# Optimization experiments

Hardware: AMD Instinct MI355X
Metric: run time of the kernel (lower is better)

The kernel has to match this reference:

```python
import jax, jax.numpy as jnp
import numpy as np

EPS = 1e-8
N_NODES, N_EDGES = 10000, 160000
SI, VI = 128, 16          # node scalar / vector channels
ES, EV = 32, 4            # edge scalar / vector channels
SO, VO = 128, 16          # output scalar / vector channels
MSI, MVI = 2 * SI + ES, 2 * VI + EV   # message input dims: 288, 36
H1 = max(MVI, VO)         # layer-1 hidden = 36 (bottleneck=1)
H2 = max(VO, VO)          # layer-2 hidden = 16
SVO = 3                   # scalarization_vectorization_output_dim


def _safe_norm(x, axis):
    return jnp.sqrt(jnp.sum(x * x, axis=axis) + EPS)


def _gcp(s, v, frames, Wdown, Wdf, Wso, bso, Wup, Wg, bg):
    """GCP block on edge-level inputs (node_inputs=False, vector_gate=True).
    s: [E, si], v: [E, vi, 3], frames: [E, 3, 3]."""
    v_pre = jnp.swapaxes(v, -1, -2)                 # [E, 3, vi]
    v_hid = v_pre @ Wdown                           # [E, 3, h]
    v_norm = _safe_norm(v_hid, axis=-2)             # [E, h]
    v_frames = v_pre @ Wdf                          # [E, 3, svo]
    # scalarize: frames @ v_frames -> [E,3,svo], transpose -> [E,svo,3], flatten to 9
    local = jnp.swapaxes(frames @ v_frames, -1, -2).reshape(v.shape[0], 3 * SVO)
    merged = jnp.concatenate([s, v_norm, local], axis=-1)
    s_out = merged @ Wso + bso                      # [E, so]
    v_out = jnp.swapaxes(v_hid @ Wup, -1, -2)       # [E, vo, 3]
    gate = jax.nn.sigmoid(jax.nn.silu(s_out) @ Wg + bg)  # vector gate
    v_out = v_out * gate[..., None]
    return jax.nn.silu(s_out), v_out


def _lin(key, fan_in, fan_out):
    return jax.random.normal(key, (fan_in, fan_out), dtype=jnp.float32) / np.sqrt(fan_in)


def setup_inputs() -> dict:
    key = jax.random.key(0)
    ks = jax.random.split(key, 24)
    M1 = H1 + MSI + 3 * SVO   # 333
    M2 = H2 + SO + 3 * SVO    # 153
    return {
        "node_s": jax.random.normal(ks[0], (N_NODES, SI), dtype=jnp.float32),
        "node_v": jax.random.normal(ks[1], (N_NODES, VI, 3), dtype=jnp.float32),
        "edge_s": jax.random.normal(ks[2], (N_EDGES, ES), dtype=jnp.float32),
        "edge_v": jax.random.normal(ks[3], (N_EDGES, EV, 3), dtype=jnp.float32),
        "frames": jax.random.normal(ks[4], (N_EDGES, 3, 3), dtype=jnp.float32),
        "g1_Wdown": _lin(ks[5], MVI, H1),
        "g1_Wdf": _lin(ks[6], MVI, SVO),
        "g1_Wso": _lin(ks[7], M1, SO),
        "g1_bso": jnp.zeros((SO,), dtype=jnp.float32),
        "g1_Wup": _lin(ks[8], H1, VO),
        "g1_Wg": _lin(ks[9], SO, VO),
        "g1_bg": jnp.zeros((VO,), dtype=jnp.float32),
        "g2_Wdown": _lin(ks[10], VO, H2),
        "g2_Wdf": _lin(ks[11], VO, SVO),
        "g2_Wso": _lin(ks[12], M2, SO),
        "g2_bso": jnp.zeros((SO,), dtype=jnp.float32),
        "g2_Wup": _lin(ks[13], H2, VO),
        "g2_Wg": _lin(ks[14], SO, VO),
        "g2_bg": jnp.zeros((VO,), dtype=jnp.float32),
        "att_W": _lin(ks[15], SO, 1),
        "att_b": jnp.zeros((1,), dtype=jnp.float32),
        "edge_index": jax.random.randint(ks[16], (2, N_EDGES), 0, N_NODES, dtype=jnp.int64),
    }


def reference(node_s, node_v, edge_s, edge_v, frames,
              g1_Wdown, g1_Wdf, g1_Wso, g1_bso, g1_Wup, g1_Wg, g1_bg,
              g2_Wdown, g2_Wdf, g2_Wso, g2_bso, g2_Wup, g2_Wg, g2_bg,
              att_W, att_b, edge_index):
    row, col = edge_index[0], edge_index[1]
    # edge gather: concat source node, edge, dest node features
    ms = jnp.concatenate([node_s[row], edge_s, node_s[col]], axis=-1)   # [E, 288]
    mv = jnp.concatenate([node_v[row], edge_v, node_v[col]], axis=1)    # [E, 36, 3]
    # message_fusion[0]
    s, v = _gcp(ms, mv, frames, g1_Wdown, g1_Wdf, g1_Wso, g1_bso, g1_Wup, g1_Wg, g1_bg)
    # message_fusion[1] with residual
    s2, v2 = _gcp(s, v, frames, g2_Wdown, g2_Wdf, g2_Wso, g2_bso, g2_Wup, g2_Wg, g2_bg)
    s, v = s + s2, v + v2
    # scalar message attention
    attn = jax.nn.sigmoid(s @ att_W + att_b)
    s = s * attn
    # flatten ScalarVector and scatter-sum aggregate to destination nodes
    flat = jnp.concatenate([s, v.reshape(v.shape[0], VO * 3)], axis=-1)  # [E, 176]
    agg = jax.ops.segment_sum(flat, row, num_segments=N_NODES)           # [N, 176]
    return agg
```

## Files before the change

### kernel.cpp

```cpp
#include <hip/hip_runtime.h>
#include <hip/hip_bf16.h>

#define E_TOT 160000
#define NN    10000
#define EPB   32

typedef unsigned short ushortT;
typedef unsigned int   uintT;
typedef __attribute__((ext_vector_type(8))) short short8;
typedef __attribute__((ext_vector_type(4))) float f32x4;

__device__ __forceinline__ float sigmoidf_(float x) { return 1.0f / (1.0f + __expf(-x)); }
__device__ __forceinline__ float siluf_(float x) { return x * sigmoidf_(x); }

__device__ __forceinline__ ushortT f2b(float f) {
    union { float f; uintT u; } x; x.f = f;
    uintT r = x.u + 0x7fffu + ((x.u >> 16) & 1u);
    return (ushortT)(r >> 16);
}
__device__ __forceinline__ float b2f(ushortT h) {
    union { uintT u; float f; } x; x.u = ((uintT)h) << 16; return x.f;
}
__device__ __forceinline__ uintT pk2(float lo, float hi) {
    union { __hip_bfloat162 h; uintT u; } cv;
    cv.h = __float22bfloat162_rn(make_float2(lo, hi));
    return cv.u;
}
__device__ __forceinline__ short8 ldfrag(const float* p) {
    const float4 x = ((const float4*)p)[0];
    const float4 y = ((const float4*)p)[1];
    union { uintT u[4]; short8 s; } r;
    r.u[0] = pk2(x.x, x.y); r.u[1] = pk2(x.z, x.w);
    r.u[2] = pk2(y.x, y.y); r.u[3] = pk2(y.z, y.w);
    return r.s;
}

#define OFF_W1SO 0
#define OFF_W2SO 45056
#define OFF_W1DF 65536
#define OFF_W1G  68608
#define OFF_W1UP 70656
#define OFF_W2DF 71680
#define OFF_W2G  72704
#define OFF_W2UP 74752
#define WT_USH   75264

#define NOFF_OFF   56320000ULL
#define CUR_OFF    56360016ULL
#define WT_OFF     57040032ULL
#define WS_CSR     57190560ULL
#define NS16_OFF   57190560ULL
#define WS_NS      59750560ULL
#define ES16_OFF   59750560ULL
#define WS_ES      69990560ULL

__device__ __forceinline__ bool idx_is64(const int* pi) {
    return (pi[1] | pi[3] | pi[5] | pi[7] | pi[9] | pi[11] | pi[13] | pi[15]) == 0;
}

__device__ __forceinline__ void weight_prep(
    int i,
    const float* __restrict__ W1so, const float* __restrict__ W2so,
    const float* __restrict__ W1d,  const float* __restrict__ W1f,
    const float* __restrict__ W1g,  const float* __restrict__ W1up,
    const float* __restrict__ W2d,  const float* __restrict__ W2f,
    const float* __restrict__ W2g,  const float* __restrict__ W2up,
    ushortT* __restrict__ ws)
{
    if (i < OFF_W2SO) {
        int n = i / 352, k = i - n * 352;
        ws[i] = (k < 333) ? f2b(W1so[k * 128 + n]) : (ushortT)0;
    } else if (i < OFF_W1DF) {
        int j = i - OFF_W2SO, n = j / 160, k = j - n * 160;
        ws[i] = (k < 153) ? f2b(W2so[k * 128 + n]) : (ushortT)0;
    } else if (i < OFF_W1G) {
        int j = i - OFF_W1DF, n = j / 64, k = j - n * 64;
        float v = 0.f;
        if (k < 36) { if (n < 36) v = W1d[k * 36 + n]; else if (n < 39) v = W1f[k * 3 + (n - 36)]; }
        ws[i] = f2b(v);
    } else if (i < OFF_W1UP) {
        int j = i - OFF_W1G, n = j / 128, k = j - n * 128;
        ws[i] = f2b(W1g[k * 16 + n]);
    } else if (i < OFF_W2DF) {
        int j = i - OFF_W1UP, n = j / 64, k = j - n * 64;
        ws[i] = (k < 36) ? f2b(W1up[k * 16 + n]) : (ushortT)0;
    } else if (i < OFF_W2G) {
        int j = i - OFF_W2DF, n = j / 32, k = j - n * 32;
        float v = 0.f;
        if (k < 16) { if (n < 16) v = W2d[k * 16 + n]; else if (n < 19) v = W2f[k * 3 + (n - 16)]; }
        ws[i] = f2b(v);
    } else if (i < OFF_W2UP) {
        int j = i - OFF_W2G, n = j / 128, k = j - n * 128;
        ws[i] = f2b(W2g[k * 16 + n]);
    } else if (i < WT_USH) {
        int j = i - OFF_W2UP, n = j / 32, k = j - n * 32;
        ws[i] = (k < 16) ? f2b(W2up[k * 16 + n]) : (ushortT)0;
    }
}

__global__ __launch_bounds__(256) void setup_kernel(
    const float* __restrict__ W1so, const float* __restrict__ W2so,
    const float* __restrict__ W1d,  const float* __restrict__ W1f,
    const float* __restrict__ W1g,  const float* __restrict__ W1up,
    const float* __restrict__ W2d,  const float* __restrict__ W2f,
    const float* __restrict__ W2g,  const float* __restrict__ W2up,
    ushortT* __restrict__ ws,
    const void* __restrict__ eidx, int* __restrict__ cur,
    const float* __restrict__ node_s, const float* __restrict__ edge_s,
    ushortT* __restrict__ ns16, ushortT* __restrict__ es16)
{
    int i = blockIdx.x * 256 + threadIdx.x;
    {
        const int* pi = (const int*)eidx;
        const long long* pl = (const long long*)eidx;
        int r = idx_is64(pi) ? (int)pl[i] : pi[i];
        atomicAdd(&cur[r], 1);
    }
    if (ns16 && i < 160000) {
        float4 x = ((const float4*)node_s)[i * 2];
        float4 y = ((const float4*)node_s)[i * 2 + 1];
        uint4 st;
        st.x = pk2(x.x, x.y); st.y = pk2(x.z, x.w);
        st.z = pk2(y.x, y.y); st.w = pk2(y.z, y.w);
        ((uint4*)ns16)[i] = st;
    }
    if (es16) {
        #pragma unroll
        for (int k = 0; k < 4; ++k) {
            float4 x = ((const float4*)edge_s)[i * 8 + 2 * k];
            float4 y = ((const float4*)edge_s)[i * 8 + 2 * k + 1];
            uint4 st;
            st.x = pk2(x.x, x.y); st.y = pk2(x.z, x.w);
            st.z = pk2(y.x, y.y); st.w = pk2(y.z, y.w);
            ((uint4*)es16)[i * 4 + k] = st;
        }
    }
    weight_prep(i, W1so, W2so, W1d, W1f, W1g, W1up, W2d, W2f, W2g, W2up, ws);
}

__global__ __launch_bounds__(256) void prep_kernel(
    const float* __restrict__ W1so, const float* __restrict__ W2so,
    const float* __restrict__ W1d,  const float* __restrict__ W1f,
    const float* __restrict__ W1g,  const float* __restrict__ W1up,
    const float* __restrict__ W2d,  const float* __restrict__ W2f,
    const float* __restrict__ W2g,  const float* __restrict__ W2up,
    ushortT* __restrict__ ws, float* __restrict__ out)
{
    int i = blockIdx.x * 256 + threadIdx.x;
    float4* o4 = (float4*)out;
    #pragma unroll
    for (int k = 0; k < 6; ++k) {
        int z = i + k * 75264;
        if (z < 440000) o4[z] = make_float4(0.f, 0.f, 0.f, 0.f);
    }
    weight_prep(i, W1so, W2so, W1d, W1f, W1g, W1up, W2d, W2f, W2g, W2up, ws);
}

__global__ __launch_bounds__(256) void scan_kernel(int* __restrict__ cur,
                                                   int* __restrict__ noff)
{
    __shared__ int buf[10000];
    __shared__ int partial[256];
    const int t = threadIdx.x;
    for (int i = t; i < NN; i += 256) buf[i] = cur[i];
    for (int i = t; i < NN; i += 256) cur[i] = 0;
    __syncthreads();
    const int base = t * 40;
    int s = 0;
    #pragma unroll
    for (int i = 0; i < 40; ++i) s += (base + i < NN) ? buf[base + i] : 0;
    partial[t] = s;
    __syncthreads();
    for (int o = 1; o < 256; o <<= 1) {
        int v = (t >= o) ? partial[t - o] : 0;
        __syncthreads();
        partial[t] += v;
        __syncthreads();
    }
    int run = (t == 0) ? 0 : partial[t - 1];
    #pragma unroll
    for (int i = 0; i < 40; ++i) {
        int gi = base + i;
        if (gi < NN) { int v = buf[gi]; noff[gi] = run; run += v; }
    }
    if (t == 255) noff[NN] = partial[255];
}

__global__ __launch_bounds__(256) void node_kernel(const ushortT* __restrict__ fb,
                                                   const int* __restrict__ noff,
                                                   float* __restrict__ out)
{
    const int w = threadIdx.x >> 6, l = threadIdx.x & 63;
    const int n = blockIdx.x * 4 + w;
    if (l >= 44) return;
    const int s = noff[n], eend = noff[n + 1];
    float a0 = 0.f, a1 = 0.f, a2 = 0.f, a3 = 0.f;
    int idx = s;
    for (; idx + 2 <= eend; idx += 2) {
        uint2 p0 = *(const uint2*)(fb + (size_t)idx * 176 + l * 4);
        uint2 p1 = *(const uint2*)(fb + (size_t)(idx + 1) * 176 + l * 4);
        a0 += b2f((ushortT)(p0.x & 0xffff)); a1 += b2f((ushortT)(p0.x >> 16));
        a2 += b2f((ushortT)(p0.y & 0xffff)); a3 += b2f((ushortT)(p0.y >> 16));
        a0 += b2f((ushortT)(p1.x & 0xffff)); a1 += b2f((ushortT)(p1.x >> 16));
        a2 += b2f((ushortT)(p1.y & 0xffff)); a3 += b2f((ushortT)(p1.y >> 16));
    }
    if (idx < eend) {
        uint2 p0 = *(const uint2*)(fb + (size_t)idx * 176 + l * 4);
        a0 += b2f((ushortT)(p0.x & 0xffff)); a1 += b2f((ushortT)(p0.x >> 16));
        a2 += b2f((ushortT)(p0.y & 0xffff)); a3 += b2f((ushortT)(p0.y >> 16));
    }
    ((float4*)(out + (size_t)n * 176))[l] = make_float4(a0, a1, a2, a3);
}

#define MFMA(a, b, c) __builtin_amdgcn_mfma_f32_16x16x32_bf16((a), (b), (c), 0, 0, 0)

__global__ __launch_bounds__(256, 5) void edge_kernel(
    const float* __restrict__ node_s, const float* __restrict__ node_v,
    const float* __restrict__ edge_s, const float* __restrict__ edge_v,
    const float* __restrict__ frames,
    const float* __restrict__ b1so, const float* __restrict__ b1g,
    const float* __restrict__ b2so, const float* __restrict__ b2g,
    const float* __restrict__ attW, const float* __restrict__ attb,
    const ushortT* __restrict__ wsc,
    const void* __restrict__ eidx, float* __restrict__ out,
    ushortT* __restrict__ fb, int* __restrict__ cur, const int* __restrict__ noff,
    const ushortT* __restrict__ ns16, const ushortT* __restrict__ es16,
    int csr)
{
    const ushortT* W1T   = wsc + OFF_W1SO;
    const ushortT* W2T   = wsc + OFF_W2SO;
    const ushortT* W1dfT = wsc + OFF_W1DF;
    const ushortT* W1gT  = wsc + OFF_W1G;
    const ushortT* W1upT = wsc + OFF_W1UP;
    const ushortT* W2dfT = wsc + OFF_W2DF;
    const ushortT* W2gT  = wsc + OFF_W2G;
    const ushortT* W2upT = wsc + OFF_W2UP;

    __shared__ __align__(16) char smem[31232];
    ushortT* mvA     = (ushortT*)smem;
    ushortT* m2      = (ushortT*)smem;
    ushortT* vhidA   = (ushortT*)(smem + 10752);
    ushortT* s2s     = (ushortT*)(smem + 10752);
    ushortT* normbuf = (ushortT*)(smem + 19456);
    ushortT* v1A     = (ushortT*)(smem + 19456);
    ushortT* vhid2A  = (ushortT*)(smem + 24064);
    float*   vfr2f   = (float*)(smem + 28672);
    float*   fr      = (float*)(smem + 29824);
    float*   attn    = (float*)(smem + 30976);
    int*     eposb   = (int*)(smem + 31104);

    const int t  = threadIdx.x;
    const int eg = blockIdx.x * EPB;
    const int w  = t >> 6, lane = t & 63, lq = lane >> 4, ln = lane & 15;
    const int te = t >> 3, tj = t & 7;
    const int p  = w & 1;

    const int* pi = (const int*)eidx;
    const long long* pl = (const long long*)eidx;
    const bool is64 = idx_is64(pi);

    {
        const int nr = is64 ? (int)pl[eg + te] : pi[eg + te];
        const int nc = is64 ? (int)pl[E_TOT + eg + te] : pi[E_TOT + eg + te];
        #pragma unroll
        for (int mi = 0; mi < 2; ++mi) {
            if (mi == 1 && tj != 0) break;
            int m = (mi == 0) ? tj : 8;
            const float* src;
            if (m < 4)       src = node_v + nr * 48 + 12 * m;
            else if (m == 4) src = edge_v + (eg + te) * 12;
            else             src = node_v + nc * 48 + 12 * (m - 5);
            float4 x = ((const float4*)src)[0];
            float4 y = ((const float4*)src)[1];
            float4 z = ((const float4*)src)[2];
            float v[12] = {x.x, x.y, x.z, x.w, y.x, y.y, y.z, y.w, z.x, z.y, z.z, z.w};
            int c0 = 4 * m;
            #pragma unroll
            for (int sp = 0; sp < 3; ++sp) {
                *(uintT*)(mvA + (sp * 32 + te) * 40 + c0)     = pk2(v[sp],     v[3 + sp]);
                *(uintT*)(mvA + (sp * 32 + te) * 40 + c0 + 2) = pk2(v[6 + sp], v[9 + sp]);
            }
        }
        #pragma unroll
        for (int k = 0; k < 2; ++k) {
            int j = tj + k * 8;
            if (j < 9) fr[te * 9 + j] = frames[(eg + te) * 9 + j];
        }
        #pragma unroll
        for (int k = 0; k < 3; ++k) {
            int c = 45 + tj + k * 8;
            if (c < 64) normbuf[te * 72 + c] = 0;
        }
        if (t < 192) {
            int r = t >> 1, cc = 36 + ((t & 1) << 1);
            *(uintT*)(mvA + r * 40 + cc) = 0;
        }
    }
    __syncthreads();

    for (int u = w; u < 18; u += 4) {
        int mt = u / 3, nt = u - mt * 3;
        const ushortT* ap = mvA + (mt * 16 + ln) * 40 + lq * 8;
        const ushortT* bp = W1dfT + (nt * 16 + ln) * 64 + lq * 8;
        f32x4 acc = {0.f, 0.f, 0.f, 0.f};
        acc = MFMA(*(const short8*)ap, *(const short8*)bp, acc);
        short8 a2 = {0, 0, 0, 0, 0, 0, 0, 0};
        if (lq == 0) a2 = *(const short8*)(ap + 32);
        acc = MFMA(a2, *(const short8*)(bp + 32), acc);
        if (nt < 2 || ln < 8) {
            ushortT* op = vhidA + (mt * 16 + lq * 4) * 40 + nt * 16 + ln;
            op[0]   = f2b(acc[0]); op[40]  = f2b(acc[1]);
            op[80]  = f2b(acc[2]); op[120] = f2b(acc[3]);
        }
    }
    __syncthreads();

    {
        #pragma unroll
        for (int k = 0; k < 5; ++k) {
            int h = tj + k * 8;
            if (h < 36) {
                float a0 = b2f(vhidA[te * 40 + h]);
                float a1 = b2f(vhidA[(32 + te) * 40 + h]);
                float a2 = b2f(vhidA[(64 + te) * 40 + h]);
                normbuf[te * 72 + h] = f2b(sqrtf(fmaf(a0, a0, fmaf(a1, a1, fmaf(a2, a2, 1e-8f)))));
            }
        }
        for (int i = t; i < 288; i += 256) {
            int e = i / 9, r = i - e * 9, a = r / 3, b = r - a * 3;
            float x = fr[e * 9 + b * 3 + 0] * b2f(vhidA[e * 40 + 36 + a])
                    + fr[e * 9 + b * 3 + 1] * b2f(vhidA[(32 + e) * 40 + 36 + a])
                    + fr[e * 9 + b * 3 + 2] * b2f(vhidA[(64 + e) * 40 + 36 + a]);
            normbuf[e * 72 + 36 + r] = f2b(x);
        }
    }
    __syncthreads();

    {
        const int klq = lq * 8;
        const int e0 = ln, e1 = 16 + ln;
        int r0, c0, r1, c1;
        if (is64) {
            r0 = (int)pl[eg + e0]; r1 = (int)pl[eg + e1];
            c0 = (int)pl[E_TOT + eg + e0]; c1 = (int)pl[E_TOT + eg + e1];
        } else {
            r0 = pi[eg + e0]; r1 = pi[eg + e1];
            c0 = pi[E_TOT + eg + e0]; c1 = pi[E_TOT + eg + e1];
        }
        r0 *= 128; c0 *= 128; r1 *= 128; c1 *= 128;
        const int eb0 = (eg + e0) * 32, eb1 = (eg + e1) * 32;
        f32x4 acc00 = {0,0,0,0}, acc01 = {0,0,0,0}, acc10 = {0,0,0,0}, acc11 = {0,0,0,0};
        const ushortT* b0p = W1T + (w * 32 + ln) * 352 + klq;
        const ushortT* b1p = W1T + (w * 32 + 16 + ln) * 352 + klq;
        #pragma unroll
        for (int ks = 0; ks < 9; ++ks) {
            short8 a0, a1;
            if (ks < 4) {
                if (ns16) {
                    a0 = *(const short8*)(ns16 + r0 + ks * 32 + klq);
                    a1 = *(const short8*)(ns16 + r1 + ks * 32 + klq);
                } else {
                    a0 = ldfrag(node_s + r0 + ks * 32 + klq);
                    a1 = ldfrag(node_s + r1 + ks * 32 + klq);
                }
            } else if (ks == 4) {
                if (es16) {
                    a0 = *(const short8*)(es16 + eb0 + klq);
                    a1 = *(const short8*)(es16 + eb1 + klq);
                } else {
                    a0 = ldfrag(edge_s + eb0 + klq);
                    a1 = ldfrag(edge_s + eb1 + klq);
                }
            } else {
                if (ns16) {
                    a0 = *(const short8*)(ns16 + c0 + (ks - 5) * 32 + klq);
                    a1 = *(const short8*)(ns16 + c1 + (ks - 5) * 32 + klq);
                } else {
                    a0 = ldfrag(node_s + c0 + (ks - 5) * 32 + klq);
                    a1 = ldfrag(node_s + c1 + (ks - 5) * 32 + klq);
                }
            }
            short8 b0 = *(const short8*)(b0p + ks * 32);
            short8 b1 = *(const short8*)(b1p + ks * 32);
            acc00 = MFMA(a0, b0, acc00); acc01 = MFMA(a0, b1, acc01);
            acc10 = MFMA(a1, b0, acc10); acc11 = MFMA(a1, b1, acc11);
        }
        #pragma unroll
        for (int ks = 9; ks < 11; ++ks) {
            short8 a0 = *(const short8*)(normbuf + e0 * 72 + (ks - 9) * 32 + klq);
            short8 a1 = *(const short8*)(normbuf + e1 * 72 + (ks - 9) * 32 + klq);
            short8 b0 = *(const short8*)(b0p + ks * 32);
            short8 b1 = *(const short8*)(b1p + ks * 32);
            acc00 = MFMA(a0, b0, acc00); acc01 = MFMA(a0, b1, acc01);
            acc10 = MFMA(a1, b0, acc10); acc11 = MFMA(a1, b1, acc11);
        }
        const int n0 = w * 32 + ln, n1 = n0 + 16;
        float bi0 = b1so[n0], bi1 = b1so[n1];
        #pragma unroll
        for (int r = 0; r < 4; ++r) {
            int m0 = lq * 4 + r;
            m2[m0 * 168 + n0]        = f2b(siluf_(acc00[r] + bi0));
            m2[m0 * 168 + n1]        = f2b(siluf_(acc01[r] + bi1));
            m2[(16 + m0) * 168 + n0] = f2b(siluf_(acc10[r] + bi0));
            m2[(16 + m0) * 168 + n1] = f2b(siluf_(acc11[r] + bi1));
        }
    }
    __syncthreads();

    {
        f32x4 gacc = {0,0,0,0};
        {
            const ushortT* ap = m2 + (p * 16 + ln) * 168;
            const ushortT* bp = W1gT + ln * 128;
            #pragma unroll
            for (int ks = 0; ks < 4; ++ks)
                gacc = MFMA(*(const short8*)(ap + ks * 32 + lq * 8),
                            *(const short8*)(bp + ks * 32 + lq * 8), gacc);
        }
        float g1[4];
        {
            float bi = b1g[ln];
            #pragma unroll
            for (int r = 0; r < 4; ++r) g1[r] = sigmoidf_(gacc[r] + bi);
        }
        const ushortT* bpu = W1upT + ln * 64 + lq * 8;
        short8 bu1 = *(const short8*)bpu;
        short8 bu2 = *(const short8*)(bpu + 32);
        #pragma unroll
        for (int c = 0; c < 2; ++c) {
            if (c == 1 && w >= 2) break;
            int mt = w + c * 4;
            const ushortT* ap = vhidA + (mt * 16 + ln) * 40 + lq * 8;
            f32x4 acc = {0,0,0,0};
            acc = MFMA(*(const short8*)ap, bu1, acc);
            short8 a2 = {0, 0, 0, 0, 0, 0, 0, 0};
            if (lq == 0) a2 = *(const short8*)(ap + 32);
            acc = MFMA(a2, bu2, acc);
            #pragma unroll
            for (int r = 0; r < 4; ++r) {
                int row = mt * 16 + lq * 4 + r;
                v1A[row * 24 + ln] = f2b(acc[r] * g1[r]);
            }
        }
        #pragma unroll
        for (int c = 0; c < 2; ++c) {
            if (c == 1 && w >= 2) break;
            int mt = w + c * 4;
            const ushortT* ap = v1A + (mt * 16 + ln) * 24 + lq * 8;
            short8 a = {0, 0, 0, 0, 0, 0, 0, 0};
            if (lq < 2) a = *(const short8*)ap;
            #pragma unroll
            for (int nt = 0; nt < 2; ++nt) {
                const ushortT* bp = W2dfT + (nt * 16 + ln) * 32 + lq * 8;
                f32x4 acc = {0,0,0,0};
                acc = MFMA(a, *(const short8*)bp, acc);
                if (nt == 0) {
                    ushortT* op = vhid2A + (mt * 16 + lq * 4) * 24 + ln;
                    op[0]  = f2b(acc[0]); op[24] = f2b(acc[1]);
                    op[48] = f2b(acc[2]); op[72] = f2b(acc[3]);
                } else if (ln < 3) {
                    float* op = vfr2f + (mt * 16 + lq * 4) * 3 + ln;
                    op[0] = acc[0]; op[3] = acc[1]; op[6] = acc[2]; op[9] = acc[3];
                }
            }
        }
    }
    __syncthreads();

    {
        #pragma unroll
        for (int k = 0; k < 2; ++k) {
            int i = t + k * 256, e = i >> 4, h = i & 15;
            float a0 = b2f(vhid2A[e * 24 + h]);
            float a1 = b2f(vhid2A[(32 + e) * 24 + h]);
            float a2 = b2f(vhid2A[(64 + e) * 24 + h]);
            m2[e * 168 + 128 + h] = f2b(sqrtf(fmaf(a0, a0, fmaf(a1, a1, fmaf(a2, a2, 1e-8f)))));
        }
        for (int i = t; i < 288; i += 256) {
            int e = i / 9, r = i - e * 9, a = r / 3, b = r - a * 3;
            float x = fr[e * 9 + b * 3 + 0] * vfr2f[e * 3 + a]
                    + fr[e * 9 + b * 3 + 1] * vfr2f[(32 + e) * 3 + a]
                    + fr[e * 9 + b * 3 + 2] * vfr2f[(64 + e) * 3 + a];
            m2[e * 168 + 144 + r] = f2b(x);
        }
        if (tj) m2[te * 168 + 152 + tj] = 0;
    }
    __syncthreads();

    {
        f32x4 acc00 = {0,0,0,0}, acc01 = {0,0,0,0}, acc10 = {0,0,0,0}, acc11 = {0,0,0,0};
        const ushortT* a0p = m2 + ln * 168 + lq * 8;
        const ushortT* a1p = m2 + (16 + ln) * 168 + lq * 8;
        const ushortT* b0p = W2T + (w * 32 + ln) * 160 + lq * 8;
        const ushortT* b1p = W2T + (w * 32 + 16 + ln) * 160 + lq * 8;
        #pragma unroll
        for (int ks = 0; ks < 5; ++ks) {
            short8 a0 = *(const short8*)(a0p + ks * 32);
            short8 a1 = *(const short8*)(a1p + ks * 32);
            short8 b0 = *(const short8*)(b0p + ks * 32);
            short8 b1 = *(const short8*)(b1p + ks * 32);
            acc00 = MFMA(a0, b0, acc00); acc01 = MFMA(a0, b1, acc01);
            acc10 = MFMA(a1, b0, acc10); acc11 = MFMA(a1, b1, acc11);
        }
        const int n0 = w * 32 + ln, n1 = n0 + 16;
        float bi0 = b2so[n0], bi1 = b2so[n1];
        #pragma unroll
        for (int r = 0; r < 4; ++r) {
            int m0 = lq * 4 + r;
            s2s[m0 * 136 + n0]        = f2b(siluf_(acc00[r] + bi0));
            s2s[m0 * 136 + n1]        = f2b(siluf_(acc01[r] + bi1));
            s2s[(16 + m0) * 136 + n0] = f2b(siluf_(acc10[r] + bi0));
            s2s[(16 + m0) * 136 + n1] = f2b(siluf_(acc11[r] + bi1));
        }
    }
    __syncthreads();

    {
        f32x4 gacc = {0,0,0,0};
        {
            const ushortT* ap = s2s + (p * 16 + ln) * 136;
            const ushortT* bp = W2gT + ln * 128;
            #pragma unroll
            for (int ks = 0; ks < 4; ++ks)
                gacc = MFMA(*(const short8*)(ap + ks * 32 + lq * 8),
                            *(const short8*)(bp + ks * 32 + lq * 8), gacc);
        }
        float g2[4];
        {
            float bi = b2g[ln];
            #pragma unroll
            for (int r = 0; r < 4; ++r) g2[r] = sigmoidf_(gacc[r] + bi);
        }
        const ushortT* bpu = W2upT + ln * 32 + lq * 8;
        short8 bu = *(const short8*)bpu;
        #pragma unroll
        for (int c = 0; c < 2; ++c) {
            if (c == 1 && w >= 2) break;
            int mt = w + c * 4;
            const ushortT* ap = vhid2A + (mt * 16 + ln) * 24 + lq * 8;
            short8 a = {0, 0, 0, 0, 0, 0, 0, 0};
            if (lq < 2) a = *(const short8*)ap;
            f32x4 acc = {0,0,0,0};
            acc = MFMA(a, bu, acc);
            #pragma unroll
            for (int r = 0; r < 4; ++r) {
                int row = mt * 16 + lq * 4 + r;
                float vfin = b2f(v1A[row * 24 + ln]) + acc[r] * g2[r];
                v1A[row * 24 + ln] = f2b(vfin);
            }
        }
        {
            float sum = 0.f;
            int c0 = tj * 16;
            #pragma unroll
            for (int c = c0; c < c0 + 16; ++c)
                sum = fmaf(b2f(m2[te * 168 + c]) + b2f(s2s[te * 136 + c]), attW[c], sum);
            sum += __shfl_xor(sum, 4);
            sum += __shfl_xor(sum, 2);
            sum += __shfl_xor(sum, 1);
            if (tj == 0) attn[te] = sigmoidf_(sum + attb[0]);
        }
        if (csr && tj == 0) {
            int nr = is64 ? (int)pl[eg + te] : pi[eg + te];
            int pos = atomicAdd(&cur[nr], 1);
            eposb[te] = noff[nr] + pos;
        }
    }
    __syncthreads();

    {
        const float at = attn[te];
        if (csr) {
            const int pos = eposb[te];
            ushortT* fbe = fb + (size_t)pos * 176;
            #pragma unroll
            for (int k = 0; k < 11; ++k) {
                int j = 2 * tj + 16 * k;
                float v0, v1;
                if (j < 128) {
                    v0 = (b2f(m2[te * 168 + j])     + b2f(s2s[te * 136 + j]))     * at;
                    v1 = (b2f(m2[te * 168 + j + 1]) + b2f(s2s[te * 136 + j + 1])) * at;
                } else {
                    int r = j - 128;
                    int o0 = r / 3,        sp0 = r - o0 * 3;
                    int o1 = (r + 1) / 3,  sp1 = (r + 1) - o1 * 3;
                    v0 = b2f(v1A[(sp0 * 32 + te) * 24 + o0]);
                    v1 = b2f(v1A[(sp1 * 32 + te) * 24 + o1]);
                }
                *(uintT*)(fbe + j) = pk2(v0, v1);
            }
        } else {
            const int nr = is64 ? (int)pl[eg + te] : pi[eg + te];
            const int orow = nr * 176;
            #pragma unroll
            for (int k = 0; k < 22; ++k) {
                int j = tj + k * 8;
                float val;
                if (j < 128) {
                    val = (b2f(m2[te * 168 + j]) + b2f(s2s[te * 136 + j])) * at;
                } else {
                    int r = j - 128, o = r / 3, sp = r - o * 3;
                    val = b2f(v1A[(sp * 32 + te) * 24 + o]);
                }
                atomicAdd(&out[orow + j], val);
            }
        }
    }
}

extern "C" void kernel_launch(void* const* d_in, const int* in_sizes, int n_in,
                              void* d_out, int out_size, void* d_ws, size_t ws_size,
                              hipStream_t stream) {
    const float* node_s = (const float*)d_in[0];
    const float* node_v = (const float*)d_in[1];
    const float* edge_s = (const float*)d_in[2];
    const float* edge_v = (const float*)d_in[3];
    const float* frames = (const float*)d_in[4];
    const float* W1d  = (const float*)d_in[5];
    const float* W1f  = (const float*)d_in[6];
    const float* W1so = (const float*)d_in[7];
    const float* b1so = (const float*)d_in[8];
    const float* W1up = (const float*)d_in[9];
    const float* W1g  = (const float*)d_in[10];
    const float* b1g  = (const float*)d_in[11];
    const float* W2d  = (const float*)d_in[12];
    const float* W2f  = (const float*)d_in[13];
    const float* W2so = (const float*)d_in[14];
    const float* b2so = (const float*)d_in[15];
    const float* W2up = (const float*)d_in[16];
    const float* W2g  = (const float*)d_in[17];
    const float* b2g  = (const float*)d_in[18];
    const float* attW = (const float*)d_in[19];
    const float* attb = (const float*)d_in[20];
    const void*  eidx = d_in[21];

    float* out = (float*)d_out;
    char* ws = (char*)d_ws;

    int mode = 0;
    if (ws_size >= WS_ES)       mode = 3;
    else if (ws_size >= WS_NS)  mode = 2;
    else if (ws_size >= WS_CSR) mode = 1;
    const int csr = (mode >= 1);

    ushortT* wt    = csr ? (ushortT*)(ws + WT_OFF)  : (ushortT*)ws;
    ushortT* fbuf  = csr ? (ushortT*)ws             : nullptr;
    int*     noff  = csr ? (int*)(ws + NOFF_OFF)    : nullptr;
    int*     cur   = csr ? (int*)(ws + CUR_OFF)     : nullptr;
    ushortT* ns16  = (mode >= 2) ? (ushortT*)(ws + NS16_OFF) : nullptr;
    ushortT* es16  = (mode >= 3) ? (ushortT*)(ws + ES16_OFF) : nullptr;

    if (csr) {
        hipMemsetAsync(cur, 0, NN * sizeof(int), stream);
        setup_kernel<<<625, 256, 0, stream>>>(
            W1so, W2so, W1d, W1f, W1g, W1up, W2d, W2f, W2g, W2up,
            wt, eidx, cur, node_s, edge_s, ns16, es16);
        scan_kernel<<<1, 256, 0, stream>>>(cur, noff);
    } else {
        prep_kernel<<<294, 256, 0, stream>>>(W1so, W2so, W1d, W1f, W1g, W1up,
                                             W2d, W2f, W2g, W2up, wt, out);
    }

    edge_kernel<<<E_TOT / EPB, 256, 0, stream>>>(
        node_s, node_v, edge_s, edge_v, frames,
        b1so, b1g, b2so, b2g, attW, attb,
        (const ushortT*)wt, eidx, out, fbuf, cur, noff, ns16, es16, csr);

    if (csr) {
        node_kernel<<<2500, 256, 0, stream>>>((const ushortT*)fbuf, noff, out);
    }
}
```

Before: 311.9 us.

## Hoist node-gather GEMM and CSR slot atomics ahead of vector-path stages

Moves the main layer-1 scalar GEMM over the gathered node and edge features (k-steps 0-8) to before the first barrier, so its global gathers overlap with the shared-memory staging, the down-projection MFMAs and the norm and frame stages. The accumulators stay live in registers across those stages, pinned with an empty asm constraint. The CSR position atomicAdd is also moved to the start of the kernel, hiding its latency earlier. The cost is higher register pressure from carrying four accumulators through the intermediate phases, which could lower occupancy.

```diff
diff --git a/kernel.cpp b/kernel.cpp
--- a/kernel.cpp
+++ b/kernel.cpp
@@ -296,48 +296,20 @@
             *(uintT*)(mvA + r * 40 + cc) = 0;
         }
     }
-    __syncthreads();
-
-    for (int u = w; u < 18; u += 4) {
-        int mt = u / 3, nt = u - mt * 3;
-        const ushortT* ap = mvA + (mt * 16 + ln) * 40 + lq * 8;
-        const ushortT* bp = W1dfT + (nt * 16 + ln) * 64 + lq * 8;
-        f32x4 acc = {0.f, 0.f, 0.f, 0.f};
-        acc = MFMA(*(const short8*)ap, *(const short8*)bp, acc);
-        short8 a2 = {0, 0, 0, 0, 0, 0, 0, 0};
-        if (lq == 0) a2 = *(const short8*)(ap + 32);
-        acc = MFMA(a2, *(const short8*)(bp + 32), acc);
-        if (nt < 2 || ln < 8) {
-            ushortT* op = vhidA + (mt * 16 + lq * 4) * 40 + nt * 16 + ln;
-            op[0]   = f2b(acc[0]); op[40]  = f2b(acc[1]);
-            op[80]  = f2b(acc[2]); op[120] = f2b(acc[3]);
-        }
-    }
-    __syncthreads();
-
-    {
-        #pragma unroll
-        for (int k = 0; k < 5; ++k) {
-            int h = tj + k * 8;
-            if (h < 36) {
-                float a0 = b2f(vhidA[te * 40 + h]);
-                float a1 = b2f(vhidA[(32 + te) * 40 + h]);
-                float a2 = b2f(vhidA[(64 + te) * 40 + h]);
-                normbuf[te * 72 + h] = f2b(sqrtf(fmaf(a0, a0, fmaf(a1, a1, fmaf(a2, a2, 1e-8f)))));
-            }
-        }
-        for (int i = t; i < 288; i += 256) {
-            int e = i / 9, r = i - e * 9, a = r / 3, b = r - a * 3;
-            float x = fr[e * 9 + b * 3 + 0] * b2f(vhidA[e * 40 + 36 + a])
-                    + fr[e * 9 + b * 3 + 1] * b2f(vhidA[(32 + e) * 40 + 36 + a])
-                    + fr[e * 9 + b * 3 + 2] * b2f(vhidA[(64 + e) * 40 + 36 + a]);
-            normbuf[e * 72 + 36 + r] = f2b(x);
-        }
-    }
-    __syncthreads();
-
-    {
-        const int klq = lq * 8;
+
+    if (csr && tj == 0) {
+        int nr = is64 ? (int)pl[eg + te] : pi[eg + te];
+        int pos = atomicAdd(&cur[nr], 1);
+        eposb[te] = noff[nr] + pos;
+    }
+
+    const int klq = lq * 8;
+    const int dn0 = w * 32 + ln, dn1 = dn0 + 16;
+    const ushortT* b0p = W1T + dn0 * 352 + klq;
+    const ushortT* b1p = W1T + dn1 * 352 + klq;
+    f32x4 acc00 = {0,0,0,0}, acc01 = {0,0,0,0}, acc10 = {0,0,0,0}, acc11 = {0,0,0,0};
+    float dbi0, dbi1;
+    {
         const int e0 = ln, e1 = 16 + ln;
         int r0, c0, r1, c1;
         if (is64) {
@@ -349,9 +321,7 @@
         }
         r0 *= 128; c0 *= 128; r1 *= 128; c1 *= 128;
         const int eb0 = (eg + e0) * 32, eb1 = (eg + e1) * 32;
-        f32x4 acc00 = {0,0,0,0}, acc01 = {0,0,0,0}, acc10 = {0,0,0,0}, acc11 = {0,0,0,0};
-        const ushortT* b0p = W1T + (w * 32 + ln) * 352 + klq;
-        const ushortT* b1p = W1T + (w * 32 + 16 + ln) * 352 + klq;
+        dbi0 = b1so[dn0]; dbi1 = b1so[dn1];
         #pragma unroll
         for (int ks = 0; ks < 9; ++ks) {
             short8 a0, a1;
@@ -385,6 +355,50 @@
             acc00 = MFMA(a0, b0, acc00); acc01 = MFMA(a0, b1, acc01);
             acc10 = MFMA(a1, b0, acc10); acc11 = MFMA(a1, b1, acc11);
         }
+    }
+    asm volatile("" : "+v"(acc00), "+v"(acc01), "+v"(acc10), "+v"(acc11));
+    __syncthreads();
+
+    for (int u = w; u < 18; u += 4) {
+        int mt = u / 3, nt = u - mt * 3;
+        const ushortT* ap = mvA + (mt * 16 + ln) * 40 + lq * 8;
+        const ushortT* bp = W1dfT + (nt * 16 + ln) * 64 + lq * 8;
+        f32x4 acc = {0.f, 0.f, 0.f, 0.f};
+        acc = MFMA(*(const short8*)ap, *(const short8*)bp, acc);
+        short8 a2 = {0, 0, 0, 0, 0, 0, 0, 0};
+        if (lq == 0) a2 = *(const short8*)(ap + 32);
+        acc = MFMA(a2, *(const short8*)(bp + 32), acc);
+        if (nt < 2 || ln < 8) {
+            ushortT* op = vhidA + (mt * 16 + lq * 4) * 40 + nt * 16 + ln;
+            op[0]   = f2b(acc[0]); op[40]  = f2b(acc[1]);
+            op[80]  = f2b(acc[2]); op[120] = f2b(acc[3]);
+        }
+    }
+    __syncthreads();
+
+    {
+        #pragma unroll
+        for (int k = 0; k < 5; ++k) {
+            int h = tj + k * 8;
+            if (h < 36) {
+                float a0 = b2f(vhidA[te * 40 + h]);
+                float a1 = b2f(vhidA[(32 + te) * 40 + h]);
+                float a2 = b2f(vhidA[(64 + te) * 40 + h]);
+                normbuf[te * 72 + h] = f2b(sqrtf(fmaf(a0, a0, fmaf(a1, a1, fmaf(a2, a2, 1e-8f)))));
+            }
+        }
+        for (int i = t; i < 288; i += 256) {
+            int e = i / 9, r = i - e * 9, a = r / 3, b = r - a * 3;
+            float x = fr[e * 9 + b * 3 + 0] * b2f(vhidA[e * 40 + 36 + a])
+                    + fr[e * 9 + b * 3 + 1] * b2f(vhidA[(32 + e) * 40 + 36 + a])
+                    + fr[e * 9 + b * 3 + 2] * b2f(vhidA[(64 + e) * 40 + 36 + a]);
+            normbuf[e * 72 + 36 + r] = f2b(x);
+        }
+    }
+    __syncthreads();
+
+    {
+        const int e0 = ln, e1 = 16 + ln;
         #pragma unroll
         for (int ks = 9; ks < 11; ++ks) {
             short8 a0 = *(const short8*)(normbuf + e0 * 72 + (ks - 9) * 32 + klq);
@@ -394,15 +408,13 @@
             acc00 = MFMA(a0, b0, acc00); acc01 = MFMA(a0, b1, acc01);
             acc10 = MFMA(a1, b0, acc10); acc11 = MFMA(a1, b1, acc11);
         }
-        const int n0 = w * 32 + ln, n1 = n0 + 16;
-        float bi0 = b1so[n0], bi1 = b1so[n1];
         #pragma unroll
         for (int r = 0; r < 4; ++r) {
             int m0 = lq * 4 + r;
-            m2[m0 * 168 + n0]        = f2b(siluf_(acc00[r] + bi0));
-            m2[m0 * 168 + n1]        = f2b(siluf_(acc01[r] + bi1));
-            m2[(16 + m0) * 168 + n0] = f2b(siluf_(acc10[r] + bi0));
-            m2[(16 + m0) * 168 + n1] = f2b(siluf_(acc11[r] + bi1));
+            m2[m0 * 168 + dn0]        = f2b(siluf_(acc00[r] + dbi0));
+            m2[m0 * 168 + dn1]        = f2b(siluf_(acc01[r] + dbi1));
+            m2[(16 + m0) * 168 + dn0] = f2b(siluf_(acc10[r] + dbi0));
+            m2[(16 + m0) * 168 + dn1] = f2b(siluf_(acc11[r] + dbi1));
         }
     }
     __syncthreads();
@@ -488,29 +500,29 @@
     __syncthreads();
 
     {
-        f32x4 acc00 = {0,0,0,0}, acc01 = {0,0,0,0}, acc10 = {0,0,0,0}, acc11 = {0,0,0,0};
+        f32x4 acc00i = {0,0,0,0}, acc01i = {0,0,0,0}, acc10i = {0,0,0,0}, acc11i = {0,0,0,0};
         const ushortT* a0p = m2 + ln * 168 + lq * 8;
         const ushortT* a1p = m2 + (16 + ln) * 168 + lq * 8;
-        const ushortT* b0p = W2T + (w * 32 + ln) * 160 + lq * 8;
-        const ushortT* b1p = W2T + (w * 32 + 16 + ln) * 160 + lq * 8;
+        const ushortT* b0pi = W2T + (w * 32 + ln) * 160 + lq * 8;
+        const ushortT* b1pi = W2T + (w * 32 + 16 + ln) * 160 + lq * 8;
         #pragma unroll
         for (int ks = 0; ks < 5; ++ks) {
             short8 a0 = *(const short8*)(a0p + ks * 32);
             short8 a1 = *(const short8*)(a1p + ks * 32);
-            short8 b0 = *(const short8*)(b0p + ks * 32);
-            short8 b1 = *(const short8*)(b1p + ks * 32);
-            acc00 = MFMA(a0, b0, acc00); acc01 = MFMA(a0, b1, acc01);
-            acc10 = MFMA(a1, b0, acc10); acc11 = MFMA(a1, b1, acc11);
+            short8 b0 = *(const short8*)(b0pi + ks * 32);
+            short8 b1 = *(const short8*)(b1pi + ks * 32);
+            acc00i = MFMA(a0, b0, acc00i); acc01i = MFMA(a0, b1, acc01i);
+            acc10i = MFMA(a1, b0, acc10i); acc11i = MFMA(a1, b1, acc11i);
         }
         const int n0 = w * 32 + ln, n1 = n0 + 16;
         float bi0 = b2so[n0], bi1 = b2so[n1];
         #pragma unroll
         for (int r = 0; r < 4; ++r) {
             int m0 = lq * 4 + r;
-            s2s[m0 * 136 + n0]        = f2b(siluf_(acc00[r] + bi0));
-            s2s[m0 * 136 + n1]        = f2b(siluf_(acc01[r] + bi1));
-            s2s[(16 + m0) * 136 + n0] = f2b(siluf_(acc10[r] + bi0));
-            s2s[(16 + m0) * 136 + n1] = f2b(siluf_(acc11[r] + bi1));
+            s2s[m0 * 136 + n0]        = f2b(siluf_(acc00i[r] + bi0));
+            s2s[m0 * 136 + n1]        = f2b(siluf_(acc01i[r] + bi1));
+            s2s[(16 + m0) * 136 + n0] = f2b(siluf_(acc10i[r] + bi0));
+            s2s[(16 + m0) * 136 + n1] = f2b(siluf_(acc11i[r] + bi1));
         }
     }
     __syncthreads();
@@ -559,11 +571,6 @@
             sum += __shfl_xor(sum, 2);
             sum += __shfl_xor(sum, 1);
             if (tj == 0) attn[te] = sigmoidf_(sum + attb[0]);
-        }
-        if (csr && tj == 0) {
-            int nr = is64 ? (int)pl[eg + te] : pi[eg + te];
-            int pos = atomicAdd(&cur[nr], 1);
-            eposb[te] = noff[nr] + pos;
         }
     }
     __syncthreads();
```

Result: no change. 312.1 us (+0.1%).
